# Kernel tuning notes

Measured on AMD Instinct MI355X. Metric: run time of the kernel, lower is better.

## Reference

```python
import jax, jax.numpy as jnp
import numpy as np

B, D, M, R, C = 1024, 32, 8, 4096, 32
TOPK_P = 0.1  # hard-coded in torch forward
EPS = 1e-9


def setup_inputs() -> dict:
    key = jax.random.key(0)
    k0, k1, k2, k3, k4 = jax.random.split(key, 5)
    x = jax.random.normal(k0, (B, D), dtype=jnp.float32)
    centers = jax.random.normal(k1, (D, M), dtype=jnp.float32)
    # widths kept away from 0 so gaussian MFs don't all underflow
    widths = jax.random.uniform(k2, (D, M), dtype=jnp.float32, minval=0.5, maxval=1.5)
    consequents = jax.random.uniform(k3, (R, D + 1, C), dtype=jnp.float32)
    rules = jax.random.randint(k4, (R, D), 0, M, dtype=jnp.int32)
    return {"x": x, "centers": centers, "widths": widths,
            "consequents": consequents, "rules": rules}


def reference(x, centers, widths, consequents, rules):
    Bn, Dn = x.shape
    Rn = rules.shape[0]
    # Gaussian membership functions: (B, D, M)
    mfs = jnp.exp(-((x[:, :, None] - centers[None]) ** 2) / (2.0 * widths[None] ** 2))
    # Gather per-rule MF values: (B, D, R)  (torch.gather along mf axis)
    rule_mfs = mfs[:, jnp.arange(Dn)[:, None], rules.T]
    # Firing strengths via product over input dims: (B, R)
    firing = jnp.prod(rule_mfs, axis=1)
    # top-K gate + scatter mask
    K = max(1, int(TOPK_P * Rn))
    _, idx = jax.lax.top_k(firing, K)
    mask = jnp.zeros_like(firing).at[jnp.arange(Bn)[:, None], idx].set(1.0)
    firing = firing * mask
    norm_fs = firing / (firing.sum(axis=1, keepdims=True) + EPS)
    # zeroG=False branch. Torch does einsum('bi,rjc->brc', x_ext, consequents)
    # which sums i and j independently: rule_mfs[b,r,c] = sum_i(x_ext[b,i]) * sum_j(cons[r,j,c]).
    # Then einsum('br,brc->bc') => out = sum(x_ext,1) * (norm_fs @ sum(cons,1)).
    x_ext_sum = x.sum(axis=1) + 1.0          # sum over x_ext = [x, 1], shape (B,)
    cons_sum = consequents.sum(axis=1)       # (R, C)
    rule_outputs = x_ext_sum[:, None] * (norm_fs @ cons_sum)  # (B, C)
    return rule_outputs, norm_fs, mask
```

## Files before the change

kernel.cpp:

```cpp
#include <hip/hip_runtime.h>

#define Bn 1024
#define Dn 32
#define Mn 8
#define Rn 4096
#define Cn 32
#define Kn 409
#define NTH 512
#define RPT 8
#define NBIN 1024
#define CCAP 256

typedef unsigned int u32;

__device__ __forceinline__ int binof(float kf) {
    int b = (int)floorf(kf * (float)(NBIN / 120.0) + (float)NBIN);
    return b < 0 ? 0 : (b > NBIN - 1 ? NBIN - 1 : b);
}

__device__ __forceinline__ float rule_sum_f32(const uint4 q, const float* __restrict__ e2) {
    float s = 0.f;
    const u32 wv[4] = {q.x, q.y, q.z, q.w};
#pragma unroll
    for (int p = 0; p < 16; ++p) {
        s += e2[(p << 6) + ((wv[p >> 2] >> (8 * (p & 3))) & 63u)];
    }
    return s;
}

__device__ __forceinline__ double rule_sum_f64(const uint4 q, const double* __restrict__ e) {
    double s = 0.0;
    const u32 wv[4] = {q.x, q.y, q.z, q.w};
#pragma unroll
    for (int p = 0; p < 16; ++p) {
        const u32 byte = (wv[p >> 2] >> (8 * (p & 3))) & 63u;
        s += e[(2 * p) * 8 + (byte & 7u)];
        s += e[(2 * p + 1) * 8 + (byte >> 3)];
    }
    return s;
}

__global__ __launch_bounds__(256) void pack_rules_kernel(const int* __restrict__ rules,
                                                         uint4* __restrict__ packed) {
    int r = blockIdx.x * 256 + threadIdx.x;
    if (r >= Rn) return;
    const int* rp = rules + r * Dn;
    u32 w[4];
#pragma unroll
    for (int wi = 0; wi < 4; ++wi) {
        u32 v = 0;
#pragma unroll
        for (int j = 0; j < 4; ++j) {
            int p = wi * 4 + j;
            u32 m0 = (u32)rp[2 * p] & 7u;
            u32 m1 = (u32)rp[2 * p + 1] & 7u;
            v |= (m0 | (m1 << 3)) << (8 * j);
        }
        w[wi] = v;
    }
    packed[r] = make_uint4(w[0], w[1], w[2], w[3]);
}

__global__ __launch_bounds__(256) void cons_sum_kernel(const float* __restrict__ cons,
                                                       float* __restrict__ out) {
    int idx = blockIdx.x * 256 + threadIdx.x;
    if (idx >= Rn * Cn) return;
    int r = idx >> 5;
    int c = idx & 31;
    const float* p = cons + (size_t)r * (Dn + 1) * Cn + c;
    float s = 0.0f;
#pragma unroll
    for (int k = 0; k < Dn + 1; ++k) s += p[(size_t)k * Cn];
    out[idx] = s;
}

__global__ __launch_bounds__(NTH, 8) void anfis_kernel(
    const float* __restrict__ x,
    const float* __restrict__ centers,
    const float* __restrict__ widths,
    const uint4* __restrict__ rpack,
    const float* __restrict__ cons_sum,
    float* __restrict__ out_rule,
    float* __restrict__ out_norm,
    float* __restrict__ out_mask)
{
    __shared__ float  s_e2[16 * 64];
    __shared__ double s_e[Dn * Mn];
    __shared__ u32    s_hist[NBIN];
    __shared__ int    s_wtot[8];
    __shared__ float  s_wsum[8];
    __shared__ int    s_cidx[CCAP];
    __shared__ double s_cval[CCAP];
    __shared__ int    s_cflag[CCAP];
    __shared__ int    s_selidx[Kn + 8];
    __shared__ float  s_selv[Kn + 8];
    __shared__ float  s_red[NTH];
    __shared__ float  s_x[Dn];
    __shared__ int    s_bb, s_nab, s_ccnt;

    const int t = threadIdx.x;
    const int lane = t & 63;
    const int w = t >> 6;
    const int b = blockIdx.x;

    if (t < Dn) s_x[t] = x[b * Dn + t];
    if (t == 0) s_ccnt = 0;
    __syncthreads();

    if (t < Dn * Mn) {
        const int d = t >> 3;
        double dx = (double)s_x[d] - (double)centers[t];
        double ww = (double)widths[t];
        s_e[t] = -(dx * dx) / (2.0 * (ww * ww));
    }
    __syncthreads();

#pragma unroll
    for (int k = t; k < 16 * 64; k += NTH) {
        int p = k >> 6, c = k & 63;
        s_e2[k] = (float)(s_e[(2 * p) * 8 + (c & 7)] + s_e[(2 * p + 1) * 8 + (c >> 3)]);
    }
    s_hist[t] = 0u;
    s_hist[t + NTH] = 0u;
    __syncthreads();

    float kf[RPT];
#pragma unroll
    for (int i = 0; i < RPT; ++i) {
        const int r = i * NTH + t;
        const float s = rule_sum_f32(rpack[r], s_e2);
        kf[i] = s;
        atomicAdd(&s_hist[binof(s)], 1u);
    }
    __syncthreads();

    const int h0 = (int)s_hist[2 * t];
    const int h1 = (int)s_hist[2 * t + 1];
    const int loc = h0 + h1;
    int S = loc;
#pragma unroll
    for (int off = 1; off < 64; off <<= 1) {
        int vv = __shfl(S, lane + off < 64 ? lane + off : lane);
        if (lane + off < 64) S += vv;
    }
    if (lane == 0) s_wtot[w] = S;
    __syncthreads();
    int wsuf = 0;
#pragma unroll
    for (int ww = 0; ww < 8; ++ww) wsuf += (ww > w) ? s_wtot[ww] : 0;
    {
        const int excl = (S - loc) + wsuf;
        const int vtot = excl + loc;
        if (excl < Kn && vtot >= Kn) {
            int c = excl;
            if (c < Kn && c + h1 >= Kn) { s_bb = 2 * t + 1; s_nab = c; }
            c += h1;
            if (c < Kn && c + h0 >= Kn) { s_bb = 2 * t; s_nab = c; }
        }
    }
    __syncthreads();
    const int bb = s_bb;
    const int want_bin = Kn - s_nab;

#pragma unroll
    for (int i = 0; i < RPT; ++i) {
        if (binof(kf[i]) == bb) {
            const int r = i * NTH + t;
            int pos = atomicAdd(&s_ccnt, 1);
            if (pos < CCAP) {
                s_cidx[pos] = r;
                s_cval[pos] = rule_sum_f64(rpack[r], s_e);
            }
        }
    }
    __syncthreads();
    const int cnt = s_ccnt < CCAP ? s_ccnt : CCAP;
    if (t < cnt) {
        const double mv = s_cval[t];
        const int mi = s_cidx[t];
        int rank = 0;
        for (int j = 0; j < cnt; ++j) {
            double ov = s_cval[j];
            int oi = s_cidx[j];
            rank += ((ov > mv) || (ov == mv && oi < mi)) ? 1 : 0;
        }
        s_cflag[t] = (rank < want_bin) ? 1 : 0;
    }
    __syncthreads();

    u32 selbits = 0u;
    int cnt_sel = 0;
    float lsum = 0.f;
#pragma unroll
    for (int i = 0; i < RPT; ++i) {
        const int r = i * NTH + t;
        const int bin = binof(kf[i]);
        bool sel = (bin > bb);
        if (bin == bb) {
            sel = false;
            for (int j = 0; j < cnt; ++j) {
                if (s_cidx[j] == r) { sel = (s_cflag[j] != 0); break; }
            }
        }
        float f = 0.f;
        if (sel) { f = expf(kf[i]); selbits |= (1u << i); ++cnt_sel; lsum += f; }
        kf[i] = f;
    }
#pragma unroll
    for (int off = 32; off >= 1; off >>= 1) lsum += __shfl_xor(lsum, off);
    if (lane == 0) s_wsum[w] = lsum;
    int p = cnt_sel;
#pragma unroll
    for (int off = 1; off < 64; off <<= 1) {
        int u = __shfl(p, lane >= off ? lane - off : lane);
        if (lane >= off) p += u;
    }
    if (lane == 63) s_wtot[w] = p;
    __syncthreads();
    float denom = 1e-9f;
#pragma unroll
    for (int ww = 0; ww < 8; ++ww) denom += s_wsum[ww];
    int base = 0;
#pragma unroll
    for (int ww = 0; ww < 8; ++ww) base += (ww < w) ? s_wtot[ww] : 0;
    int pos = base + (p - cnt_sel);

    float* onorm = out_norm + (size_t)b * Rn;
    float* omask = out_mask + (size_t)b * Rn;
#pragma unroll
    for (int i = 0; i < RPT; ++i) {
        const int r = i * NTH + t;
        const bool sel = (selbits >> i) & 1u;
        float nv = 0.f;
        if (sel) {
            nv = kf[i] / denom;
            s_selidx[pos] = r;
            s_selv[pos] = nv;
            ++pos;
        }
        onorm[r] = nv;
        omask[r] = sel ? 1.f : 0.f;
    }
    __syncthreads();

    const int g = t >> 5;
    const int c = t & 31;
    float acc = 0.f;
    for (int i = g; i < Kn; i += 16) {
        acc += s_selv[i] * cons_sum[s_selidx[i] * Cn + c];
    }
    s_red[t] = acc;
    __syncthreads();
    if (t < Cn) {
        float ss = 0.f;
#pragma unroll
        for (int gg = 0; gg < 16; ++gg) ss += s_red[gg * 32 + t];
        float xs = 1.f;
#pragma unroll
        for (int d = 0; d < Dn; ++d) xs += s_x[d];
        out_rule[b * Cn + t] = xs * ss;
    }
}

extern "C" void kernel_launch(void* const* d_in, const int* in_sizes, int n_in,
                              void* d_out, int out_size, void* d_ws, size_t ws_size,
                              hipStream_t stream) {
    (void)in_sizes; (void)n_in; (void)out_size; (void)ws_size;
    const float* x = (const float*)d_in[0];
    const float* centers = (const float*)d_in[1];
    const float* widths = (const float*)d_in[2];
    const float* consequents = (const float*)d_in[3];
    const int* rules = (const int*)d_in[4];

    float* out_rule = (float*)d_out;
    float* out_norm = out_rule + (size_t)Bn * Cn;
    float* out_mask = out_norm + (size_t)Bn * Rn;

    float* cons_sum = (float*)d_ws;
    uint4* rpack = (uint4*)((char*)d_ws + (size_t)Rn * Cn * sizeof(float));

    pack_rules_kernel<<<Rn / 256, 256, 0, stream>>>(rules, rpack);
    cons_sum_kernel<<<(Rn * Cn) / 256, 256, 0, stream>>>(consequents, cons_sum);
    anfis_kernel<<<Bn, NTH, 0, stream>>>(x, centers, widths, rpack, cons_sum,
                                         out_rule, out_norm, out_mask);
}
```

Measured before the change: 50.67 us.

## Fuse prep kernels, compute rule sums via wave shuffles, track candidate positions

Merges the rule-packing and consequent-sum kernels into one launch so there is one fewer kernel launch. The pairwise exponent table now lives in registers and is read with cross-lane shuffles instead of LDS, which drops a barrier and the s_e2 table. Candidate rules remember their slot index, so the linear search over candidates is no longer needed. Launch bounds drop to 4 waves per SIMD to make room for the extra registers. Each rule lookup now costs 16 shuffles, and these may be slower than LDS reads.

```diff
diff --git a/kernel.cpp b/kernel.cpp
--- a/kernel.cpp
+++ b/kernel.cpp
@@ -18,16 +18,6 @@
     return b < 0 ? 0 : (b > NBIN - 1 ? NBIN - 1 : b);
 }
 
-__device__ __forceinline__ float rule_sum_f32(const uint4 q, const float* __restrict__ e2) {
-    float s = 0.f;
-    const u32 wv[4] = {q.x, q.y, q.z, q.w};
-#pragma unroll
-    for (int p = 0; p < 16; ++p) {
-        s += e2[(p << 6) + ((wv[p >> 2] >> (8 * (p & 3))) & 63u)];
-    }
-    return s;
-}
-
 __device__ __forceinline__ double rule_sum_f64(const uint4 q, const double* __restrict__ e) {
     double s = 0.0;
     const u32 wv[4] = {q.x, q.y, q.z, q.w};
@@ -40,41 +30,43 @@
     return s;
 }
 
-__global__ __launch_bounds__(256) void pack_rules_kernel(const int* __restrict__ rules,
-                                                         uint4* __restrict__ packed) {
-    int r = blockIdx.x * 256 + threadIdx.x;
-    if (r >= Rn) return;
-    const int* rp = rules + r * Dn;
-    u32 w[4];
-#pragma unroll
-    for (int wi = 0; wi < 4; ++wi) {
-        u32 v = 0;
-#pragma unroll
-        for (int j = 0; j < 4; ++j) {
-            int p = wi * 4 + j;
-            u32 m0 = (u32)rp[2 * p] & 7u;
-            u32 m1 = (u32)rp[2 * p + 1] & 7u;
-            v |= (m0 | (m1 << 3)) << (8 * j);
-        }
-        w[wi] = v;
-    }
-    packed[r] = make_uint4(w[0], w[1], w[2], w[3]);
-}
-
-__global__ __launch_bounds__(256) void cons_sum_kernel(const float* __restrict__ cons,
-                                                       float* __restrict__ out) {
-    int idx = blockIdx.x * 256 + threadIdx.x;
-    if (idx >= Rn * Cn) return;
-    int r = idx >> 5;
-    int c = idx & 31;
-    const float* p = cons + (size_t)r * (Dn + 1) * Cn + c;
-    float s = 0.0f;
-#pragma unroll
-    for (int k = 0; k < Dn + 1; ++k) s += p[(size_t)k * Cn];
-    out[idx] = s;
-}
-
-__global__ __launch_bounds__(NTH, 8) void anfis_kernel(
+__global__ __launch_bounds__(256) void prep_kernel(const float* __restrict__ cons,
+                                                   const int* __restrict__ rules,
+                                                   float* __restrict__ cons_out,
+                                                   uint4* __restrict__ packed) {
+    const int blk = blockIdx.x;
+    const int t = threadIdx.x;
+    if (blk < (Rn * Cn) / 256) {
+        int idx = blk * 256 + t;
+        int r = idx >> 5;
+        int c = idx & 31;
+        const float* p = cons + (size_t)r * (Dn + 1) * Cn + c;
+        float s = 0.0f;
+#pragma unroll
+        for (int k = 0; k < Dn + 1; ++k) s += p[(size_t)k * Cn];
+        cons_out[idx] = s;
+    } else {
+        int r = (blk - (Rn * Cn) / 256) * 256 + t;
+        if (r >= Rn) return;
+        const int* rp = rules + r * Dn;
+        u32 w[4];
+#pragma unroll
+        for (int wi = 0; wi < 4; ++wi) {
+            u32 v = 0;
+#pragma unroll
+            for (int j = 0; j < 4; ++j) {
+                int p = wi * 4 + j;
+                u32 m0 = (u32)rp[2 * p] & 7u;
+                u32 m1 = (u32)rp[2 * p + 1] & 7u;
+                v |= (m0 | (m1 << 3)) << (8 * j);
+            }
+            w[wi] = v;
+        }
+        packed[r] = make_uint4(w[0], w[1], w[2], w[3]);
+    }
+}
+
+__global__ __launch_bounds__(NTH, 4) void anfis_kernel(
     const float* __restrict__ x,
     const float* __restrict__ centers,
     const float* __restrict__ widths,
@@ -84,7 +76,7 @@
     float* __restrict__ out_norm,
     float* __restrict__ out_mask)
 {
-    __shared__ float  s_e2[16 * 64];
+    __shared__ float  s_x[Dn];
     __shared__ double s_e[Dn * Mn];
     __shared__ u32    s_hist[NBIN];
     __shared__ int    s_wtot[8];
@@ -95,7 +87,6 @@
     __shared__ int    s_selidx[Kn + 8];
     __shared__ float  s_selv[Kn + 8];
     __shared__ float  s_red[NTH];
-    __shared__ float  s_x[Dn];
     __shared__ int    s_bb, s_nab, s_ccnt;
 
     const int t = threadIdx.x;
@@ -105,6 +96,8 @@
 
     if (t < Dn) s_x[t] = x[b * Dn + t];
     if (t == 0) s_ccnt = 0;
+    s_hist[t] = 0u;
+    s_hist[t + NTH] = 0u;
     __syncthreads();
 
     if (t < Dn * Mn) {
@@ -113,22 +106,37 @@
         double ww = (double)widths[t];
         s_e[t] = -(dx * dx) / (2.0 * (ww * ww));
     }
-    __syncthreads();
-
-#pragma unroll
-    for (int k = t; k < 16 * 64; k += NTH) {
-        int p = k >> 6, c = k & 63;
-        s_e2[k] = (float)(s_e[(2 * p) * 8 + (c & 7)] + s_e[(2 * p + 1) * 8 + (c >> 3)]);
-    }
-    s_hist[t] = 0u;
-    s_hist[t + NTH] = 0u;
-    __syncthreads();
+
+    float ereg[4];
+#pragma unroll
+    for (int j = 0; j < 4; ++j) {
+        const int idx = j * 64 + lane;
+        const int d = idx >> 3;
+        float dx = s_x[d] - centers[idx];
+        float ww = widths[idx];
+        ereg[j] = -(dx * dx) / (2.0f * ww * ww);
+    }
+    float e2r[16];
+#pragma unroll
+    for (int p = 0; p < 16; ++p) {
+        const int s0 = (16 * p) & 63;
+        const int s1 = (16 * p + 8) & 63;
+        e2r[p] = __shfl(ereg[p >> 2], s0 + (lane & 7)) +
+                 __shfl(ereg[p >> 2], s1 + (lane >> 3));
+    }
 
     float kf[RPT];
 #pragma unroll
     for (int i = 0; i < RPT; ++i) {
         const int r = i * NTH + t;
-        const float s = rule_sum_f32(rpack[r], s_e2);
+        const uint4 q = rpack[r];
+        const u32 wv[4] = {q.x, q.y, q.z, q.w};
+        float s = 0.f;
+#pragma unroll
+        for (int p = 0; p < 16; ++p) {
+            const int byte = (int)((wv[p >> 2] >> (8 * (p & 3))) & 63u);
+            s += __shfl(e2r[p], byte);
+        }
         kf[i] = s;
         atomicAdd(&s_hist[binof(s)], 1u);
     }
@@ -162,12 +170,15 @@
     const int bb = s_bb;
     const int want_bin = Kn - s_nab;
 
-#pragma unroll
-    for (int i = 0; i < RPT; ++i) {
+    int mypos[RPT];
+#pragma unroll
+    for (int i = 0; i < RPT; ++i) {
+        mypos[i] = -1;
         if (binof(kf[i]) == bb) {
             const int r = i * NTH + t;
             int pos = atomicAdd(&s_ccnt, 1);
             if (pos < CCAP) {
+                mypos[i] = pos;
                 s_cidx[pos] = r;
                 s_cval[pos] = rule_sum_f64(rpack[r], s_e);
             }
@@ -193,15 +204,8 @@
     float lsum = 0.f;
 #pragma unroll
     for (int i = 0; i < RPT; ++i) {
-        const int r = i * NTH + t;
-        const int bin = binof(kf[i]);
-        bool sel = (bin > bb);
-        if (bin == bb) {
-            sel = false;
-            for (int j = 0; j < cnt; ++j) {
-                if (s_cidx[j] == r) { sel = (s_cflag[j] != 0); break; }
-            }
-        }
+        bool sel = (binof(kf[i]) > bb);
+        if (mypos[i] >= 0) sel = (s_cflag[mypos[i]] != 0);
         float f = 0.f;
         if (sel) { f = expf(kf[i]); selbits |= (1u << i); ++cnt_sel; lsum += f; }
         kf[i] = f;
@@ -279,8 +283,8 @@
     float* cons_sum = (float*)d_ws;
     uint4* rpack = (uint4*)((char*)d_ws + (size_t)Rn * Cn * sizeof(float));
 
-    pack_rules_kernel<<<Rn / 256, 256, 0, stream>>>(rules, rpack);
-    cons_sum_kernel<<<(Rn * Cn) / 256, 256, 0, stream>>>(consequents, cons_sum);
+    const int prep_blocks = (Rn * Cn) / 256 + (Rn + 255) / 256;
+    prep_kernel<<<prep_blocks, 256, 0, stream>>>(consequents, rules, cons_sum, rpack);
     anfis_kernel<<<Bn, NTH, 0, stream>>>(x, centers, widths, rpack, cons_sum,
                                          out_rule, out_norm, out_mask);
 }
```

New measurement: 55.81 us. 1.1x slower.
